# Performance work log

Hardware: AMD Instinct MI355X
Metric: run time of the kernel (lower is better)

The kernel has to match this reference:

```python
import jax, jax.numpy as jnp
import numpy as np
from jax import lax

THRESH_WIDTH = 20  # default thresh_width in soft_skeletonize
SMOOTH = 1.0


def _max_pool3(x):
    # 3x3 max pool, stride 1, padding 1 (torch pads with -inf for max pool)
    return lax.reduce_window(x, -jnp.inf, lax.max,
                             (1, 1, 3, 3), (1, 1, 1, 1),
                             [(0, 0), (0, 0), (1, 1), (1, 1)])


def _soft_skeletonize(x):
    def body(i, x):
        min_pool_x = -_max_pool3(-x)
        contour = jax.nn.relu(_max_pool3(min_pool_x) - min_pool_x)
        return jax.nn.relu(x - contour)
    return lax.fori_loop(0, THRESH_WIDTH, body, x)


def _norm_intersection(center_line, vessel):
    clf = center_line.ravel()
    vf = vessel.ravel()
    intersection = jnp.sum(clf * vf)
    return (intersection + SMOOTH) / (jnp.sum(clf) + SMOOTH)


def setup_inputs() -> dict:
    key = jax.random.key(0)
    k1, k2 = jax.random.split(key)
    shape = (16, 1, 1024, 1024)
    pred = jax.random.uniform(k1, shape, dtype=jnp.float32)
    gt = jax.random.uniform(k2, shape, dtype=jnp.float32)
    return {"pred": pred, "gt": gt}


def reference(pred, gt):
    # channel == 1 path: pred used as-is (float)
    pred = pred.astype(jnp.float32)
    cl_pred = _soft_skeletonize(pred)
    target_skeleton = _soft_skeletonize(gt)
    iflat = _norm_intersection(cl_pred, gt)
    tflat = _norm_intersection(target_skeleton, pred)
    intersection = iflat * tflat
    loss = 1.0 - 2.0 * intersection / (iflat + tflat)
    return loss  # scalar; .squeeze() in torch is a no-op here
```

## Files before the change

### kernel.cpp

```cpp
#include <hip/hip_runtime.h>
#include <math.h>


#define IMG_H 1024
#define IMG_W 1024
#define IMG_N (IMG_H * IMG_W)
#define NIMG  16
#define NZ    32
#define BH    64
#define NBANDS (IMG_H / BH)
#define K     4
#define EW    258
#define NBLK  (NZ * NBANDS)
#define NITER (BH + 6 * K)

typedef _Float16 h2 __attribute__((ext_vector_type(2)));

__device__ __forceinline__ h2 hmin2(h2 a, h2 b) { return __builtin_elementwise_min(a, b); }
__device__ __forceinline__ h2 hmax2(h2 a, h2 b) { return __builtin_elementwise_max(a, b); }

union U32H { unsigned u; h2 h; };
__device__ __forceinline__ unsigned as_u(h2 h) { U32H t; t.h = h; return t.u; }
__device__ __forceinline__ h2 as_h2(unsigned u) { U32H t; t.u = u; return t.h; }

struct Hp { h2 lo, hi; };
struct St { Hp hm1, hm2, m2, m3, q1, q2, x1, x2, x3, xc; };

template<int MASKED>
__device__ __forceinline__ Hp stage_step(
    St& s, h2 rmask, int t, const uint2 (&e2)[EW])
{
    h2 lp = as_h2(e2[t].y);
    h2 rp = as_h2(e2[t + 2].x);
    h2 midx = (h2){s.xc.lo[1], s.xc.hi[0]};
    h2 hlo = hmin2(hmin2((h2){lp[0], s.xc.lo[0]}, s.xc.lo), midx);
    h2 hhi = hmin2(hmin2(midx, s.xc.hi), (h2){s.xc.hi[1], rp[0]});
    h2 mlo, mhi;
    if constexpr (MASKED) {
        mlo = hmin2(hmin2(hmin2(s.hm1.lo, s.hm2.lo), hlo), rmask);
        mhi = hmin2(hmin2(hmin2(s.hm1.hi, s.hm2.hi), hhi), rmask);
    } else {
        mlo = hmin2(hmin2(s.hm1.lo, s.hm2.lo), hlo);
        mhi = hmin2(hmin2(s.hm1.hi, s.hm2.hi), hhi);
    }
    h2 midm = (h2){s.m2.lo[1], s.m2.hi[0]};
    h2 qlo = hmax2(hmax2((h2){lp[1], s.m2.lo[0]}, s.m2.lo), midm);
    h2 qhi = hmax2(hmax2(midm, s.m2.hi), (h2){s.m2.hi[1], rp[1]});
    h2 Mlo = hmax2(hmax2(s.q1.lo, s.q2.lo), qlo);
    h2 Mhi = hmax2(hmax2(s.q1.hi, s.q2.hi), qhi);
    const h2 Z2 = (h2){(_Float16)0.f, (_Float16)0.f};
    h2 elo = hmax2(s.x3.lo - hmax2(Mlo - s.m3.lo, Z2), Z2);
    h2 ehi = hmax2(s.x3.hi - hmax2(Mhi - s.m3.hi, Z2), Z2);
    s.hm1 = s.hm2; s.hm2.lo = hlo; s.hm2.hi = hhi;
    s.m3  = s.m2;  s.m2.lo  = mlo; s.m2.hi  = mhi;
    s.q1  = s.q2;  s.q2.lo  = qlo; s.q2.hi  = qhi;
    s.x3  = s.x2;  s.x2 = s.x1;    s.x1 = s.xc;
    Hp e; e.lo = elo; e.hi = ehi;
    return e;
}

template<int FIRST, int MASKED>
__device__ __forceinline__ Hp load_row(
    int y, int c, const float* __restrict__ f32src,
    const unsigned short* __restrict__ bsrc)
{
    const _Float16 HINF = (_Float16)__builtin_huge_valf();
    Hp x; x.lo = (h2){HINF, HINF}; x.hi = (h2){HINF, HINF};
    if (!MASKED || (unsigned)y < (unsigned)IMG_H) {
        if constexpr (FIRST) {
            float4 f = *(const float4*)(f32src + (size_t)y * IMG_W + c);
            x.lo = (h2){(_Float16)f.x, (_Float16)f.y};
            x.hi = (h2){(_Float16)f.z, (_Float16)f.w};
        } else {
            uint2 u = *(const uint2*)(bsrc + (size_t)y * IMG_W + c);
            x.lo = as_h2(u.x);
            x.hi = as_h2(u.y);
        }
    }
    return x;
}

template<int FIRST, int LAST, int MASKED>
__device__ __forceinline__ void iter_step(
    int y, int t, int c, int r0, St (&st)[K], Hp& xn,
    const float* __restrict__ f32src, const unsigned short* __restrict__ bsrc,
    unsigned short* __restrict__ bdst, const float* __restrict__ oth,
    float& a1, float& a2, uint2 (&e2)[K][EW])
{
    const _Float16 HINF = (_Float16)__builtin_huge_valf();
    const h2 PINF2 = (h2){HINF, HINF};
    const h2 NINF2 = (h2){-HINF, -HINF};

    Hp tnext = load_row<FIRST, MASKED>(y + 2, c, f32src, bsrc);

    __syncthreads();

    h2 rm = PINF2;
    if constexpr (MASKED)
        rm = ((unsigned)(y - (4 * (K - 1) + 1)) < (unsigned)IMG_H) ? PINF2 : NINF2;
    Hp eK = stage_step<MASKED>(st[K - 1], rm, t, e2[K - 1]);
    #pragma unroll
    for (int k = K - 2; k >= 0; --k) {
        if constexpr (MASKED)
            rm = ((unsigned)(y - 4 * k - 1) < (unsigned)IMG_H) ? PINF2 : NINF2;
        Hp e = stage_step<MASKED>(st[k], rm, t, e2[k]);
        if constexpr (MASKED) {
            h2 em = ((unsigned)(y - 4 * k - 3) < (unsigned)IMG_H) ? NINF2 : PINF2;
            st[k + 1].xc.lo = hmax2(e.lo, em);
            st[k + 1].xc.hi = hmax2(e.hi, em);
        } else {
            st[k + 1].xc = e;
        }
    }
    st[0].xc = xn;
    xn = tnext;

    __syncthreads();

    #pragma unroll
    for (int k = 0; k < K; ++k) {
        e2[k][t + 1] = make_uint2(
            as_u((h2){st[k].xc.lo[0], st[k].m2.lo[0]}),
            as_u((h2){st[k].xc.hi[1], st[k].m2.hi[1]}));
    }

    int orow = y - (4 * (K - 1) + 3);
    if ((unsigned)(orow - r0) < (unsigned)BH) {
        if constexpr (!LAST) {
            *(uint2*)(bdst + (size_t)orow * IMG_W + c) =
                make_uint2(as_u(eK.lo), as_u(eK.hi));
        } else {
            float4 ov = *(const float4*)(oth + (size_t)orow * IMG_W + c);
            float e0 = (float)eK.lo[0], e1 = (float)eK.lo[1];
            float e2f = (float)eK.hi[0], e3 = (float)eK.hi[1];
            a1 += e0 * ov.x + e1 * ov.y + e2f * ov.z + e3 * ov.w;
            a2 += e0 + e1 + e2f + e3;
        }
    }
}

template<int FIRST, int LAST>
__global__ __launch_bounds__(256, 1) void skel(
    const unsigned short* __restrict__ src, unsigned short* __restrict__ dst,
    const float* __restrict__ pred32, const float* __restrict__ gt32,
    double* __restrict__ partials)
{
    __shared__ uint2 e2[K][EW];
    __shared__ double l1[4], l2[4];

    const int t = threadIdx.x, c = 4 * t;
    const int band = blockIdx.x, z = blockIdx.y;
    const int r0 = band * BH;
    const _Float16 HINF = (_Float16)__builtin_huge_valf();
    const h2 PINF2 = (h2){HINF, HINF};
    const h2 NINF2 = (h2){-HINF, -HINF};

    const float* f32src = (z < NIMG) ? pred32 + (size_t)z * IMG_N
                                     : gt32 + (size_t)(z - NIMG) * IMG_N;
    const unsigned short* bsrc = FIRST ? nullptr : src + (size_t)z * IMG_N;
    unsigned short* bdst = LAST ? nullptr : dst + (size_t)z * IMG_N;
    const float* oth = LAST ? ((z < NIMG) ? gt32 + (size_t)z * IMG_N
                                          : pred32 + (size_t)(z - NIMG) * IMG_N)
                            : nullptr;

    if (t < K) {
        e2[t][0]      = make_uint2(0u, 0xFC007C00u);
        e2[t][EW - 1] = make_uint2(0xFC007C00u, 0u);
    }

    St st[K];
    #pragma unroll
    for (int k = 0; k < K; ++k) {
        st[k].hm1.lo = st[k].hm1.hi = PINF2;
        st[k].hm2.lo = st[k].hm2.hi = PINF2;
        st[k].m2.lo  = st[k].m2.hi  = NINF2;
        st[k].m3.lo  = st[k].m3.hi  = NINF2;
        st[k].q1.lo  = st[k].q1.hi  = NINF2;
        st[k].q2.lo  = st[k].q2.hi  = NINF2;
        st[k].x1.lo  = st[k].x1.hi  = PINF2;
        st[k].x2.lo  = st[k].x2.hi  = PINF2;
        st[k].x3.lo  = st[k].x3.hi  = PINF2;
        st[k].xc.lo  = st[k].xc.hi  = PINF2;
    }

    const int y0 = r0 - 2 * K;
    st[0].xc = load_row<FIRST, 1>(y0, c, f32src, bsrc);
    Hp xn    = load_row<FIRST, 1>(y0 + 1, c, f32src, bsrc);

    #pragma unroll
    for (int k = 0; k < K; ++k) {
        e2[k][t + 1] = make_uint2(
            as_u((h2){st[k].xc.lo[0], st[k].m2.lo[0]}),
            as_u((h2){st[k].xc.hi[1], st[k].m2.hi[1]}));
    }

    float a1 = 0.f, a2 = 0.f;
    if (band >= 1 && band <= NBANDS - 2) {
        #pragma unroll 4
        for (int i = 0; i < NITER; ++i)
            iter_step<FIRST, LAST, 0>(y0 + i, t, c, r0, st, xn, f32src, bsrc, bdst, oth, a1, a2, e2);
    } else {
        #pragma unroll 4
        for (int i = 0; i < NITER; ++i)
            iter_step<FIRST, LAST, 1>(y0 + i, t, c, r0, st, xn, f32src, bsrc, bdst, oth, a1, a2, e2);
    }

    if constexpr (LAST) {
        double d1 = a1, d2 = a2;
        for (int off = 32; off; off >>= 1) {
            d1 += __shfl_down(d1, off);
            d2 += __shfl_down(d2, off);
        }
        const int w = t >> 6;
        if ((t & 63) == 0) { l1[w] = d1; l2[w] = d2; }
        __syncthreads();
        if (t == 0) {
            int bid = z * NBANDS + band;
            partials[2 * bid]     = l1[0] + l1[1] + l1[2] + l1[3];
            partials[2 * bid + 1] = l2[0] + l2[1] + l2[2] + l2[3];
        }
    }
}

__global__ __launch_bounds__(256) void finalize(
    const double* __restrict__ pp, float* __restrict__ out)
{
    __shared__ double sh[4][4];
    double i1 = 0, i2 = 0, t1 = 0, t2 = 0;
    for (int i = threadIdx.x; i < NBLK; i += 256) {
        double a = pp[2 * i], b = pp[2 * i + 1];
        if (i < NIMG * NBANDS) { i1 += a; i2 += b; }
        else                   { t1 += a; t2 += b; }
    }
    for (int off = 32; off; off >>= 1) {
        i1 += __shfl_down(i1, off); i2 += __shfl_down(i2, off);
        t1 += __shfl_down(t1, off); t2 += __shfl_down(t2, off);
    }
    const int w = threadIdx.x >> 6;
    if ((threadIdx.x & 63) == 0) { sh[0][w] = i1; sh[1][w] = i2; sh[2][w] = t1; sh[3][w] = t2; }
    __syncthreads();
    if (threadIdx.x == 0) {
        double s1 = 0, s2 = 0, s3 = 0, s4 = 0;
        for (int j = 0; j < 4; ++j) { s1 += sh[0][j]; s2 += sh[1][j]; s3 += sh[2][j]; s4 += sh[3][j]; }
        double iflat = (s1 + 1.0) / (s2 + 1.0);
        double tflat = (s3 + 1.0) / (s4 + 1.0);
        out[0] = (float)(1.0 - 2.0 * (iflat * tflat) / (iflat + tflat));
    }
}

extern "C" void kernel_launch(void* const* d_in, const int* in_sizes, int n_in,
                              void* d_out, int out_size, void* d_ws, size_t ws_size,
                              hipStream_t stream)
{
    const float* pred = (const float*)d_in[0];
    const float* gt   = (const float*)d_in[1];

    unsigned short* A = (unsigned short*)d_ws;
    unsigned short* B = A + (size_t)NZ * IMG_N;
    double* partials  = (double*)d_ws;
    dim3 grid(NBANDS, NZ);

    skel<1, 0><<<grid, 256, 0, stream>>>(nullptr, A, pred, gt, nullptr);
    skel<0, 0><<<grid, 256, 0, stream>>>(A, B, pred, gt, nullptr);
    skel<0, 0><<<grid, 256, 0, stream>>>(B, A, pred, gt, nullptr);
    skel<0, 0><<<grid, 256, 0, stream>>>(A, B, pred, gt, nullptr);
    skel<0, 1><<<grid, 256, 0, stream>>>(B, nullptr, pred, gt, partials);

    finalize<<<1, 256, 0, stream>>>(partials, (float*)d_out);
}
```

Measured before the change: 559.6 us.

## Process pred and gt images together in each block for more ILP

Each block now runs the four-stage skeleton pipeline for two images at once, the pred image and the matching gt image, which halves the grid to 256 blocks. The two independent chains are interleaved inside one iteration, so each barrier is shared by twice the work and the independent instructions can hide latency. The cost is doubled register state (two sets of St[K]) and doubled shared memory per block. With launch_bounds(256,1) and only 256 blocks, this risks register spills and leaves a large GPU like MI355X with fewer blocks than it has CUs.

```diff
diff --git a/kernel.cpp b/kernel.cpp
--- a/kernel.cpp
+++ b/kernel.cpp
@@ -11,7 +11,7 @@
 #define NBANDS (IMG_H / BH)
 #define K     4
 #define EW    258
-#define NBLK  (NZ * NBANDS)
+#define NPART (NZ * NBANDS)
 #define NITER (BH + 6 * K)
 
 typedef _Float16 h2 __attribute__((ext_vector_type(2)));
@@ -82,59 +82,70 @@
 
 template<int FIRST, int LAST, int MASKED>
 __device__ __forceinline__ void iter_step(
-    int y, int t, int c, int r0, St (&st)[K], Hp& xn,
-    const float* __restrict__ f32src, const unsigned short* __restrict__ bsrc,
-    unsigned short* __restrict__ bdst, const float* __restrict__ oth,
-    float& a1, float& a2, uint2 (&e2)[K][EW])
+    int y, int t, int c, int r0, St (&st)[2][K], Hp (&xn)[2],
+    const float* const (&f32src)[2], const unsigned short* const (&bsrc)[2],
+    unsigned short* const (&bdst)[2], const float* const (&oth)[2],
+    float (&acc)[4], uint2 (&e2)[2][K][EW])
 {
     const _Float16 HINF = (_Float16)__builtin_huge_valf();
     const h2 PINF2 = (h2){HINF, HINF};
     const h2 NINF2 = (h2){-HINF, -HINF};
 
-    Hp tnext = load_row<FIRST, MASKED>(y + 2, c, f32src, bsrc);
+    Hp tnext[2];
+    #pragma unroll
+    for (int im = 0; im < 2; ++im)
+        tnext[im] = load_row<FIRST, MASKED>(y + 2, c, f32src[im], bsrc[im]);
 
     __syncthreads();
 
-    h2 rm = PINF2;
-    if constexpr (MASKED)
-        rm = ((unsigned)(y - (4 * (K - 1) + 1)) < (unsigned)IMG_H) ? PINF2 : NINF2;
-    Hp eK = stage_step<MASKED>(st[K - 1], rm, t, e2[K - 1]);
-    #pragma unroll
-    for (int k = K - 2; k >= 0; --k) {
+    Hp eK[2];
+    #pragma unroll
+    for (int im = 0; im < 2; ++im) {
+        h2 rm = PINF2;
         if constexpr (MASKED)
-            rm = ((unsigned)(y - 4 * k - 1) < (unsigned)IMG_H) ? PINF2 : NINF2;
-        Hp e = stage_step<MASKED>(st[k], rm, t, e2[k]);
-        if constexpr (MASKED) {
-            h2 em = ((unsigned)(y - 4 * k - 3) < (unsigned)IMG_H) ? NINF2 : PINF2;
-            st[k + 1].xc.lo = hmax2(e.lo, em);
-            st[k + 1].xc.hi = hmax2(e.hi, em);
-        } else {
-            st[k + 1].xc = e;
-        }
-    }
-    st[0].xc = xn;
-    xn = tnext;
+            rm = ((unsigned)(y - (4 * (K - 1) + 1)) < (unsigned)IMG_H) ? PINF2 : NINF2;
+        eK[im] = stage_step<MASKED>(st[im][K - 1], rm, t, e2[im][K - 1]);
+        #pragma unroll
+        for (int k = K - 2; k >= 0; --k) {
+            if constexpr (MASKED)
+                rm = ((unsigned)(y - 4 * k - 1) < (unsigned)IMG_H) ? PINF2 : NINF2;
+            Hp e = stage_step<MASKED>(st[im][k], rm, t, e2[im][k]);
+            if constexpr (MASKED) {
+                h2 em = ((unsigned)(y - 4 * k - 3) < (unsigned)IMG_H) ? NINF2 : PINF2;
+                st[im][k + 1].xc.lo = hmax2(e.lo, em);
+                st[im][k + 1].xc.hi = hmax2(e.hi, em);
+            } else {
+                st[im][k + 1].xc = e;
+            }
+        }
+        st[im][0].xc = xn[im];
+        xn[im] = tnext[im];
+    }
 
     __syncthreads();
 
     #pragma unroll
-    for (int k = 0; k < K; ++k) {
-        e2[k][t + 1] = make_uint2(
-            as_u((h2){st[k].xc.lo[0], st[k].m2.lo[0]}),
-            as_u((h2){st[k].xc.hi[1], st[k].m2.hi[1]}));
-    }
+    for (int im = 0; im < 2; ++im)
+        #pragma unroll
+        for (int k = 0; k < K; ++k)
+            e2[im][k][t + 1] = make_uint2(
+                as_u((h2){st[im][k].xc.lo[0], st[im][k].m2.lo[0]}),
+                as_u((h2){st[im][k].xc.hi[1], st[im][k].m2.hi[1]}));
 
     int orow = y - (4 * (K - 1) + 3);
     if ((unsigned)(orow - r0) < (unsigned)BH) {
-        if constexpr (!LAST) {
-            *(uint2*)(bdst + (size_t)orow * IMG_W + c) =
-                make_uint2(as_u(eK.lo), as_u(eK.hi));
-        } else {
-            float4 ov = *(const float4*)(oth + (size_t)orow * IMG_W + c);
-            float e0 = (float)eK.lo[0], e1 = (float)eK.lo[1];
-            float e2f = (float)eK.hi[0], e3 = (float)eK.hi[1];
-            a1 += e0 * ov.x + e1 * ov.y + e2f * ov.z + e3 * ov.w;
-            a2 += e0 + e1 + e2f + e3;
+        #pragma unroll
+        for (int im = 0; im < 2; ++im) {
+            if constexpr (!LAST) {
+                *(uint2*)(bdst[im] + (size_t)orow * IMG_W + c) =
+                    make_uint2(as_u(eK[im].lo), as_u(eK[im].hi));
+            } else {
+                float4 ov = *(const float4*)(oth[im] + (size_t)orow * IMG_W + c);
+                float e0 = (float)eK[im].lo[0], e1 = (float)eK[im].lo[1];
+                float e2f = (float)eK[im].hi[0], e3 = (float)eK[im].hi[1];
+                acc[2 * im]     += e0 * ov.x + e1 * ov.y + e2f * ov.z + e3 * ov.w;
+                acc[2 * im + 1] += e0 + e1 + e2f + e3;
+            }
         }
     }
 }
@@ -145,8 +156,8 @@
     const float* __restrict__ pred32, const float* __restrict__ gt32,
     double* __restrict__ partials)
 {
-    __shared__ uint2 e2[K][EW];
-    __shared__ double l1[4], l2[4];
+    __shared__ uint2 e2[2][K][EW];
+    __shared__ double lsum[4][4];
 
     const int t = threadIdx.x, c = 4 * t;
     const int band = blockIdx.x, z = blockIdx.y;
@@ -155,69 +166,94 @@
     const h2 PINF2 = (h2){HINF, HINF};
     const h2 NINF2 = (h2){-HINF, -HINF};
 
-    const float* f32src = (z < NIMG) ? pred32 + (size_t)z * IMG_N
-                                     : gt32 + (size_t)(z - NIMG) * IMG_N;
-    const unsigned short* bsrc = FIRST ? nullptr : src + (size_t)z * IMG_N;
-    unsigned short* bdst = LAST ? nullptr : dst + (size_t)z * IMG_N;
-    const float* oth = LAST ? ((z < NIMG) ? gt32 + (size_t)z * IMG_N
-                                          : pred32 + (size_t)(z - NIMG) * IMG_N)
-                            : nullptr;
+    const float* f32src[2] = { pred32 + (size_t)z * IMG_N,
+                               gt32   + (size_t)z * IMG_N };
+    const unsigned short* bsrc[2] = {
+        FIRST ? nullptr : src + (size_t)z * IMG_N,
+        FIRST ? nullptr : src + (size_t)(z + NIMG) * IMG_N };
+    unsigned short* bdst[2] = {
+        LAST ? nullptr : dst + (size_t)z * IMG_N,
+        LAST ? nullptr : dst + (size_t)(z + NIMG) * IMG_N };
+    const float* oth[2] = {
+        LAST ? gt32   + (size_t)z * IMG_N : nullptr,
+        LAST ? pred32 + (size_t)z * IMG_N : nullptr };
 
     if (t < K) {
-        e2[t][0]      = make_uint2(0u, 0xFC007C00u);
-        e2[t][EW - 1] = make_uint2(0xFC007C00u, 0u);
-    }
-
-    St st[K];
-    #pragma unroll
-    for (int k = 0; k < K; ++k) {
-        st[k].hm1.lo = st[k].hm1.hi = PINF2;
-        st[k].hm2.lo = st[k].hm2.hi = PINF2;
-        st[k].m2.lo  = st[k].m2.hi  = NINF2;
-        st[k].m3.lo  = st[k].m3.hi  = NINF2;
-        st[k].q1.lo  = st[k].q1.hi  = NINF2;
-        st[k].q2.lo  = st[k].q2.hi  = NINF2;
-        st[k].x1.lo  = st[k].x1.hi  = PINF2;
-        st[k].x2.lo  = st[k].x2.hi  = PINF2;
-        st[k].x3.lo  = st[k].x3.hi  = PINF2;
-        st[k].xc.lo  = st[k].xc.hi  = PINF2;
-    }
+        #pragma unroll
+        for (int im = 0; im < 2; ++im) {
+            e2[im][t][0]      = make_uint2(0u, 0xFC007C00u);
+            e2[im][t][EW - 1] = make_uint2(0xFC007C00u, 0u);
+        }
+    }
+
+    St st[2][K];
+    #pragma unroll
+    for (int im = 0; im < 2; ++im)
+        #pragma unroll
+        for (int k = 0; k < K; ++k) {
+            st[im][k].hm1.lo = st[im][k].hm1.hi = PINF2;
+            st[im][k].hm2.lo = st[im][k].hm2.hi = PINF2;
+            st[im][k].m2.lo  = st[im][k].m2.hi  = NINF2;
+            st[im][k].m3.lo  = st[im][k].m3.hi  = NINF2;
+            st[im][k].q1.lo  = st[im][k].q1.hi  = NINF2;
+            st[im][k].q2.lo  = st[im][k].q2.hi  = NINF2;
+            st[im][k].x1.lo  = st[im][k].x1.hi  = PINF2;
+            st[im][k].x2.lo  = st[im][k].x2.hi  = PINF2;
+            st[im][k].x3.lo  = st[im][k].x3.hi  = PINF2;
+            st[im][k].xc.lo  = st[im][k].xc.hi  = PINF2;
+        }
 
     const int y0 = r0 - 2 * K;
-    st[0].xc = load_row<FIRST, 1>(y0, c, f32src, bsrc);
-    Hp xn    = load_row<FIRST, 1>(y0 + 1, c, f32src, bsrc);
-
-    #pragma unroll
-    for (int k = 0; k < K; ++k) {
-        e2[k][t + 1] = make_uint2(
-            as_u((h2){st[k].xc.lo[0], st[k].m2.lo[0]}),
-            as_u((h2){st[k].xc.hi[1], st[k].m2.hi[1]}));
-    }
-
-    float a1 = 0.f, a2 = 0.f;
+    Hp xn[2];
+    #pragma unroll
+    for (int im = 0; im < 2; ++im) {
+        st[im][0].xc = load_row<FIRST, 1>(y0, c, f32src[im], bsrc[im]);
+        xn[im]       = load_row<FIRST, 1>(y0 + 1, c, f32src[im], bsrc[im]);
+    }
+
+    #pragma unroll
+    for (int im = 0; im < 2; ++im)
+        #pragma unroll
+        for (int k = 0; k < K; ++k)
+            e2[im][k][t + 1] = make_uint2(
+                as_u((h2){st[im][k].xc.lo[0], st[im][k].m2.lo[0]}),
+                as_u((h2){st[im][k].xc.hi[1], st[im][k].m2.hi[1]}));
+
+    float acc[4] = {0.f, 0.f, 0.f, 0.f};
     if (band >= 1 && band <= NBANDS - 2) {
         #pragma unroll 4
         for (int i = 0; i < NITER; ++i)
-            iter_step<FIRST, LAST, 0>(y0 + i, t, c, r0, st, xn, f32src, bsrc, bdst, oth, a1, a2, e2);
+            iter_step<FIRST, LAST, 0>(y0 + i, t, c, r0, st, xn, f32src, bsrc, bdst, oth, acc, e2);
     } else {
         #pragma unroll 4
         for (int i = 0; i < NITER; ++i)
-            iter_step<FIRST, LAST, 1>(y0 + i, t, c, r0, st, xn, f32src, bsrc, bdst, oth, a1, a2, e2);
+            iter_step<FIRST, LAST, 1>(y0 + i, t, c, r0, st, xn, f32src, bsrc, bdst, oth, acc, e2);
     }
 
     if constexpr (LAST) {
-        double d1 = a1, d2 = a2;
+        double d[4] = {acc[0], acc[1], acc[2], acc[3]};
         for (int off = 32; off; off >>= 1) {
-            d1 += __shfl_down(d1, off);
-            d2 += __shfl_down(d2, off);
+            #pragma unroll
+            for (int j = 0; j < 4; ++j)
+                d[j] += __shfl_down(d[j], off);
         }
         const int w = t >> 6;
-        if ((t & 63) == 0) { l1[w] = d1; l2[w] = d2; }
+        if ((t & 63) == 0) {
+            #pragma unroll
+            for (int j = 0; j < 4; ++j) lsum[j][w] = d[j];
+        }
         __syncthreads();
         if (t == 0) {
-            int bid = z * NBANDS + band;
-            partials[2 * bid]     = l1[0] + l1[1] + l1[2] + l1[3];
-            partials[2 * bid + 1] = l2[0] + l2[1] + l2[2] + l2[3];
+            double s[4];
+            #pragma unroll
+            for (int j = 0; j < 4; ++j)
+                s[j] = lsum[j][0] + lsum[j][1] + lsum[j][2] + lsum[j][3];
+            int bid0 = z * NBANDS + band;
+            int bid1 = (z + NIMG) * NBANDS + band;
+            partials[2 * bid0]     = s[0];
+            partials[2 * bid0 + 1] = s[1];
+            partials[2 * bid1]     = s[2];
+            partials[2 * bid1 + 1] = s[3];
         }
     }
 }
@@ -227,7 +263,7 @@
 {
     __shared__ double sh[4][4];
     double i1 = 0, i2 = 0, t1 = 0, t2 = 0;
-    for (int i = threadIdx.x; i < NBLK; i += 256) {
+    for (int i = threadIdx.x; i < NPART; i += 256) {
         double a = pp[2 * i], b = pp[2 * i + 1];
         if (i < NIMG * NBANDS) { i1 += a; i2 += b; }
         else                   { t1 += a; t2 += b; }
@@ -258,7 +294,7 @@
     unsigned short* A = (unsigned short*)d_ws;
     unsigned short* B = A + (size_t)NZ * IMG_N;
     double* partials  = (double*)d_ws;
-    dim3 grid(NBANDS, NZ);
+    dim3 grid(NBANDS, NIMG);
 
     skel<1, 0><<<grid, 256, 0, stream>>>(nullptr, A, pred, gt, nullptr);
     skel<0, 0><<<grid, 256, 0, stream>>>(A, B, pred, gt, nullptr);
```

Result: slower. 727.9 us (+30.1%).
